# Performance work log

Measured on AMD Instinct MI355X. Metric: run time of the kernel, lower is better.

Reference implementation:

```python
import jax, jax.numpy as jnp
import numpy as np
import math

HEAD_DIM = 128

def _rope(t, cos, sin):
    # t: [B, S, H, D]; cos/sin: [S, D//2]; rotates consecutive pairs (view_as_complex semantics)
    B, S, H, D = t.shape
    t2 = t.reshape(B, S, H, D // 2, 2)
    t0, t1 = t2[..., 0], t2[..., 1]
    c = cos[None, :, None, :]
    s = sin[None, :, None, :]
    r0 = t0 * c - t1 * s
    r1 = t0 * s + t1 * c
    return jnp.stack([r0, r1], axis=-1).reshape(B, S, H, D)

def setup_inputs() -> dict:
    key = jax.random.key(0)
    ks = jax.random.split(key, 8)
    B, S, dim = 32, 1, 4096
    n_q, n_kv, hd = 32, 8, HEAD_DIM
    max_seq = 2048
    start_pos = 2047
    x = jax.random.normal(ks[0], (B, S, dim), dtype=jnp.float32)
    wq = jax.random.normal(ks[1], (n_q * hd, dim), dtype=jnp.float32) * 0.02
    wk = jax.random.normal(ks[2], (n_kv * hd, dim), dtype=jnp.float32) * 0.02
    wv = jax.random.normal(ks[3], (n_kv * hd, dim), dtype=jnp.float32) * 0.02
    wo = jax.random.normal(ks[4], (dim, n_q * hd), dtype=jnp.float32) * 0.02
    # real RoPE frequencies at positions [start_pos, start_pos+S)
    inv_freq = 1.0 / (10000.0 ** (np.arange(0, hd, 2, dtype=np.float32) / hd))  # [hd//2]
    pos = np.arange(start_pos, start_pos + S, dtype=np.float32)[:, None]
    angles = pos * inv_freq[None, :]  # [S, hd//2]
    freqs_cos = jnp.asarray(np.cos(angles), dtype=jnp.float32)
    freqs_sin = jnp.asarray(np.sin(angles), dtype=jnp.float32)
    cache_k = jax.random.normal(ks[5], (B, max_seq, n_kv, hd), dtype=jnp.float32)
    cache_v = jax.random.normal(ks[6], (B, max_seq, n_kv, hd), dtype=jnp.float32)
    return {"x": x, "wq": wq, "wk": wk, "wv": wv, "wo": wo,
            "freqs_cos": freqs_cos, "freqs_sin": freqs_sin,
            "cache_k": cache_k, "cache_v": cache_v, "start_pos": start_pos}

def reference(x, wq, wk, wv, wo, freqs_cos, freqs_sin, cache_k, cache_v, start_pos):
    B, S, dim = x.shape
    hd = HEAD_DIM
    n_q = wq.shape[0] // hd
    n_kv = wk.shape[0] // hd
    rep = n_q // n_kv
    q = (x @ wq.T).reshape(B, S, n_q, hd)
    k = (x @ wk.T).reshape(B, S, n_kv, hd)
    v = (x @ wv.T).reshape(B, S, n_kv, hd)
    q = _rope(q, freqs_cos, freqs_sin)
    k = _rope(k, freqs_cos, freqs_sin)
    # KV-cache update (start_pos is a static Python int)
    ck = jax.lax.dynamic_update_slice(cache_k, k, (0, start_pos, 0, 0))
    cv = jax.lax.dynamic_update_slice(cache_v, v, (0, start_pos, 0, 0))
    T = start_pos + S
    kk = ck[:, :T]  # [B, T, n_kv, hd]
    vv = cv[:, :T]
    # GQA without materializing repeated heads: q head h -> (g=h//rep, r=h%rep)
    qg = q.reshape(B, S, n_kv, rep, hd)
    scores = jnp.einsum('bsgrd,btgd->bgrst', qg, kk) / math.sqrt(hd)
    attn = jax.nn.softmax(scores, axis=-1)
    out = jnp.einsum('bgrst,btgd->bsgrd', attn, vv).reshape(B, S, n_q * hd)
    return out @ wo.T
```

## Files before the change

### kernel.cpp

```cpp
#include <hip/hip_runtime.h>
#include <hip/hip_bf16.h>


typedef __bf16 bf16x8_t __attribute__((ext_vector_type(8)));
typedef float f32x4_t __attribute__((ext_vector_type(4)));

#define KDIM 4096
#define NTOT_QKV 6144
#define NTOT_O 4096
#define NKV 8
#define HD 128

static __device__ inline bf16x8_t cvt8(const float4* p) {
  float4 u = p[0], v = p[1];
  bf16x8_t r;
  r[0] = (__bf16)u.x; r[1] = (__bf16)u.y; r[2] = (__bf16)u.z; r[3] = (__bf16)u.w;
  r[4] = (__bf16)v.x; r[5] = (__bf16)v.y; r[6] = (__bf16)v.z; r[7] = (__bf16)v.w;
  return r;
}

__global__ __launch_bounds__(256) void qkv_mfma(
    const float* __restrict__ X,
    const float* __restrict__ Wq,
    const float* __restrict__ Wk,
    const float* __restrict__ Wv,
    float* __restrict__ part)
{
  int wid  = (blockIdx.x * blockDim.x + threadIdx.x) >> 6;
  int lane = threadIdx.x & 63;
  const int ntiles = NTOT_QKV >> 4;
  int nt = wid % ntiles;
  int kc = wid / ntiles;
  int k0 = kc << 9;
  int rr = lane & 15;
  int quad = lane >> 4;

  int ng = nt * 16 + rr;
  const float* Wrow;
  if (ng < 4096)      Wrow = Wq + (size_t)ng * KDIM;
  else if (ng < 5120) Wrow = Wk + (size_t)(ng - 4096) * KDIM;
  else                Wrow = Wv + (size_t)(ng - 5120) * KDIM;

  const float4* pa0 = (const float4*)(X + (size_t)rr * KDIM + k0) + quad * 2;
  const float4* pa1 = (const float4*)(X + (size_t)(rr + 16) * KDIM + k0) + quad * 2;
  const float4* pbv = (const float4*)(Wrow + k0) + quad * 2;

  f32x4_t acc0 = {0.f, 0.f, 0.f, 0.f};
  f32x4_t acc1 = {0.f, 0.f, 0.f, 0.f};
  #pragma unroll 4
  for (int s = 0; s < 16; ++s) {
    bf16x8_t a0 = cvt8(pa0 + s * 8);
    bf16x8_t a1 = cvt8(pa1 + s * 8);
    bf16x8_t bb = cvt8(pbv + s * 8);
    acc0 = __builtin_amdgcn_mfma_f32_16x16x32_bf16(a0, bb, acc0, 0, 0, 0);
    acc1 = __builtin_amdgcn_mfma_f32_16x16x32_bf16(a1, bb, acc1, 0, 0, 0);
  }
  float* p = part + (size_t)kc * 32 * NTOT_QKV + ng;
  #pragma unroll
  for (int i = 0; i < 4; ++i) {
    int m = quad * 4 + i;
    p[(size_t)m * NTOT_QKV] = acc0[i];
    p[(size_t)(m + 16) * NTOT_QKV] = acc1[i];
  }
}

__global__ __launch_bounds__(256) void reduce_rope(
    const float* __restrict__ part,
    const float* __restrict__ cosv,
    const float* __restrict__ sinv,
    float* __restrict__ qws,
    float* __restrict__ kws,
    float* __restrict__ vws)
{
  int idx = blockIdx.x * blockDim.x + threadIdx.x;
  int b = idx / 3072;
  int rem = idx - b * 3072;
  int n0 = rem * 2;
  const float* p = part + (size_t)b * NTOT_QKV + n0;
  float s0 = 0.f, s1 = 0.f;
  #pragma unroll
  for (int c = 0; c < 8; ++c) {
    s0 += p[(size_t)c * 32 * NTOT_QKV + 0];
    s1 += p[(size_t)c * 32 * NTOT_QKV + 1];
  }
  if (n0 < 4096) {
    int d = n0 & 127; int j = d >> 1;
    float cf = cosv[j], sf = sinv[j];
    qws[(size_t)b * 4096 + n0]     = s0 * cf - s1 * sf;
    qws[(size_t)b * 4096 + n0 + 1] = s0 * sf + s1 * cf;
  } else if (n0 < 5120) {
    int nn = n0 - 4096;
    int d = nn & 127; int j = d >> 1;
    float cf = cosv[j], sf = sinv[j];
    kws[(size_t)b * 1024 + nn]     = s0 * cf - s1 * sf;
    kws[(size_t)b * 1024 + nn + 1] = s0 * sf + s1 * cf;
  } else {
    int nn = n0 - 5120;
    vws[(size_t)b * 1024 + nn]     = s0;
    vws[(size_t)b * 1024 + nn + 1] = s1;
  }
}

__global__ __launch_bounds__(256) void attn_partial(
    const float* __restrict__ cache_k,
    const float* __restrict__ cache_v,
    const float* __restrict__ qws,
    const float* __restrict__ kws,
    const float* __restrict__ vws,
    float* __restrict__ part)
{
  int bidx = blockIdx.x;
  int c = bidx & 7;
  int pair = bidx >> 3;
  int h = pair & 7, b = pair >> 3;
  int tid = threadIdx.x;

  __shared__ float4 kbuf[2048];
  __shared__ float4 q4l[128];
  __shared__ float4 pl4[256];

  if (tid < 128)
    q4l[tid] = ((const float4*)(qws + (size_t)b * 4096 + (size_t)h * 512))[tid];

  const int r  = tid >> 6;
  const int tl = tid & 63;
  const int sw = tl & 7;

  float s[4];
  #pragma unroll
  for (int st = 0; st < 4; ++st) {
    int t0 = c * 256 + st * 64;
    float4 tmp[8];
    #pragma unroll
    for (int j = 0; j < 8; ++j) {
      int f = tid + j * 256;
      int row = f >> 5, col = f & 31;
      const float4* src;
      if (c == 7 && st == 3 && row == 63)
        src = (const float4*)(kws + ((size_t)b * NKV + h) * HD) + col;
      else
        src = (const float4*)(cache_k + (((size_t)b * 2048 + t0 + row) * NKV + h) * HD) + col;
      tmp[j] = *src;
    }
    #pragma unroll
    for (int j = 0; j < 8; ++j) {
      int f = tid + j * 256;
      int row = f >> 5, col = f & 31;
      kbuf[row * 32 + (col ^ (row & 7))] = tmp[j];
    }
    __syncthreads();
    const float4* kr = kbuf + tl * 32;
    float acc = 0.f;
    #pragma unroll 8
    for (int d4 = 0; d4 < 32; ++d4) {
      float4 q4 = q4l[r * 32 + d4];
      float4 k4 = kr[d4 ^ sw];
      acc += q4.x * k4.x + q4.y * k4.y + q4.z * k4.z + q4.w * k4.w;
    }
    s[st] = acc * 0.088388347648318447f;
    __syncthreads();
  }

  float m = fmaxf(fmaxf(s[0], s[1]), fmaxf(s[2], s[3]));
  #pragma unroll
  for (int off = 32; off; off >>= 1) m = fmaxf(m, __shfl_xor(m, off, 64));
  float lsum = 0.f;
  float* plf = (float*)pl4;
  #pragma unroll
  for (int st = 0; st < 4; ++st) {
    float p = __expf(s[st] - m);
    lsum += p;
    plf[(st * 64 + tl) * 4 + r] = p;
  }
  #pragma unroll
  for (int off = 32; off; off >>= 1) lsum += __shfl_xor(lsum, off, 64);

  float* pb = part + (size_t)bidx * 520;
  if (tl == 0) { pb[r] = m; pb[4 + r] = lsum; }
  __syncthreads();

  int d4 = tid & 31;
  int g  = tid >> 3 >> 2;
  float4 a0 = {0,0,0,0}, a1 = {0,0,0,0}, a2 = {0,0,0,0}, a3 = {0,0,0,0};
  const float4* vp = (const float4*)(cache_v +
      (((size_t)b * 2048 + c * 256 + g * 32) * NKV + h) * HD) + d4;
  #pragma unroll 4
  for (int i = 0; i < 32; ++i) {
    float4 v4 = vp[(size_t)i * 256];
    float4 pv = pl4[g * 32 + i];
    a0.x += pv.x * v4.x; a0.y += pv.x * v4.y; a0.z += pv.x * v4.z; a0.w += pv.x * v4.w;
    a1.x += pv.y * v4.x; a1.y += pv.y * v4.y; a1.z += pv.y * v4.z; a1.w += pv.y * v4.w;
    a2.x += pv.z * v4.x; a2.y += pv.z * v4.y; a2.z += pv.z * v4.z; a2.w += pv.z * v4.w;
    a3.x += pv.w * v4.x; a3.y += pv.w * v4.y; a3.z += pv.w * v4.z; a3.w += pv.w * v4.w;
  }
  if (c == 7 && g == 7) {
    float4 vold = vp[(size_t)31 * 256];
    float4 vn = ((const float4*)(vws + ((size_t)b * NKV + h) * HD))[d4];
    float4 dv; dv.x = vn.x - vold.x; dv.y = vn.y - vold.y;
    dv.z = vn.z - vold.z; dv.w = vn.w - vold.w;
    float4 pv = pl4[255];
    a0.x += pv.x * dv.x; a0.y += pv.x * dv.y; a0.z += pv.x * dv.z; a0.w += pv.x * dv.w;
    a1.x += pv.y * dv.x; a1.y += pv.y * dv.y; a1.z += pv.y * dv.z; a1.w += pv.y * dv.w;
    a2.x += pv.z * dv.x; a2.y += pv.z * dv.y; a2.z += pv.z * dv.z; a2.w += pv.z * dv.w;
    a3.x += pv.w * dv.x; a3.y += pv.w * dv.y; a3.z += pv.w * dv.z; a3.w += pv.w * dv.w;
  }
  float4* pred = kbuf;
  pred[(g * 4 + 0) * 32 + d4] = a0;
  pred[(g * 4 + 1) * 32 + d4] = a1;
  pred[(g * 4 + 2) * 32 + d4] = a2;
  pred[(g * 4 + 3) * 32 + d4] = a3;
  __syncthreads();

  if (tid < 128) {
    int r2 = tid >> 5, dd = tid & 31;
    float4 o = {0,0,0,0};
    #pragma unroll
    for (int gg = 0; gg < 8; ++gg) {
      float4 t4 = pred[(gg * 4 + r2) * 32 + dd];
      o.x += t4.x; o.y += t4.y; o.z += t4.z; o.w += t4.w;
    }
    *(float4*)(pb + 8 + r2 * 128 + dd * 4) = o;
  }
}

__global__ __launch_bounds__(128) void attn_combine(
    const float* __restrict__ part,
    float* __restrict__ attn_out)
{
  int pair = blockIdx.x;
  int h = pair & 7, b = pair >> 3;
  int d = threadIdx.x;
  const float* pb = part + (size_t)pair * 8 * 520;
  #pragma unroll
  for (int r = 0; r < 4; ++r) {
    float M = -1e30f;
    #pragma unroll
    for (int c = 0; c < 8; ++c) M = fmaxf(M, pb[c * 520 + r]);
    float L = 0.f, o = 0.f;
    #pragma unroll
    for (int c = 0; c < 8; ++c) {
      float w = __expf(pb[c * 520 + r] - M);
      L += w * pb[c * 520 + 4 + r];
      o += w * pb[c * 520 + 8 + r * 128 + d];
    }
    attn_out[(size_t)b * 4096 + (h * 4 + r) * 128 + d] = o / L;
  }
}

__global__ __launch_bounds__(256) void oproj_mfma(
    const float* __restrict__ X,
    const float* __restrict__ W,
    float* __restrict__ part)
{
  int wid  = (blockIdx.x * blockDim.x + threadIdx.x) >> 6;
  int lane = threadIdx.x & 63;
  const int ntiles = NTOT_O >> 4;
  int nt = wid % ntiles;
  int kc = wid / ntiles;
  int k0 = kc << 9;
  int rr = lane & 15;
  int quad = lane >> 4;
  int ng = nt * 16 + rr;

  const float4* pa0 = (const float4*)(X + (size_t)rr * KDIM + k0) + quad * 2;
  const float4* pa1 = (const float4*)(X + (size_t)(rr + 16) * KDIM + k0) + quad * 2;
  const float4* pbv = (const float4*)(W + (size_t)ng * KDIM + k0) + quad * 2;

  f32x4_t acc0 = {0.f, 0.f, 0.f, 0.f};
  f32x4_t acc1 = {0.f, 0.f, 0.f, 0.f};
  #pragma unroll 4
  for (int s = 0; s < 16; ++s) {
    bf16x8_t a0 = cvt8(pa0 + s * 8);
    bf16x8_t a1 = cvt8(pa1 + s * 8);
    bf16x8_t bb = cvt8(pbv + s * 8);
    acc0 = __builtin_amdgcn_mfma_f32_16x16x32_bf16(a0, bb, acc0, 0, 0, 0);
    acc1 = __builtin_amdgcn_mfma_f32_16x16x32_bf16(a1, bb, acc1, 0, 0, 0);
  }
  float* p = part + (size_t)kc * 32 * NTOT_O + ng;
  #pragma unroll
  for (int i = 0; i < 4; ++i) {
    int m = quad * 4 + i;
    p[(size_t)m * NTOT_O] = acc0[i];
    p[(size_t)(m + 16) * NTOT_O] = acc1[i];
  }
}

__global__ __launch_bounds__(256) void oproj_reduce(
    const float* __restrict__ part,
    float* __restrict__ out)
{
  int i = blockIdx.x * blockDim.x + threadIdx.x;
  float s = 0.f;
  #pragma unroll
  for (int c = 0; c < 8; ++c) s += part[(size_t)c * 131072 + i];
  out[i] = s;
}

extern "C" void kernel_launch(void* const* d_in, const int* in_sizes, int n_in,
                              void* d_out, int out_size, void* d_ws, size_t ws_size,
                              hipStream_t stream) {
  const float* x  = (const float*)d_in[0];
  const float* wq = (const float*)d_in[1];
  const float* wk = (const float*)d_in[2];
  const float* wv = (const float*)d_in[3];
  const float* wo = (const float*)d_in[4];
  const float* fc = (const float*)d_in[5];
  const float* fs = (const float*)d_in[6];
  const float* ck = (const float*)d_in[7];
  const float* cv = (const float*)d_in[8];

  char* ws = (char*)d_ws;
  float* part_qkv = (float*)(ws + 0);
  float* qws      = (float*)(ws + 6291456);
  float* kws      = (float*)(ws + 6815744);
  float* vws      = (float*)(ws + 6946816);
  float* part_at  = (float*)(ws + 7077888);
  float* attn_out = (float*)(ws + 11337728);
  float* part_o   = (float*)(ws + 0);

  qkv_mfma<<<768, 256, 0, stream>>>(x, wq, wk, wv, part_qkv);
  reduce_rope<<<384, 256, 0, stream>>>(part_qkv, fc, fs, qws, kws, vws);
  attn_partial<<<2048, 256, 0, stream>>>(ck, cv, qws, kws, vws, part_at);
  attn_combine<<<256, 128, 0, stream>>>(part_at, attn_out);
  oproj_mfma<<<512, 256, 0, stream>>>(attn_out, wo, part_o);
  oproj_reduce<<<512, 256, 0, stream>>>(part_o, (float*)d_out);
}
```

Measured before the change: 642.7 us.

## Pre-cast activations to bf16, double-buffer weight tiles in LDS, prefetch K cache

Adds a cast_x kernel and has attn_combine write bf16, so both GEMMs read bf16 activations instead of converting fp32 in every wave. The QKV and O-projection GEMMs now give each block a 64-column tile and stage converted weights through a double-buffered, swizzled LDS tile. The next K-step's global loads are issued before the current MFMAs, so load latency overlaps with compute. The attention kernel similarly prefetches the next K-cache tile into registers while computing on the current one. The costs are one extra kernel launch, more barriers, and higher register and LDS use.

```diff
diff --git a/kernel.cpp b/kernel.cpp
--- a/kernel.cpp
+++ b/kernel.cpp
@@ -11,50 +11,96 @@
 #define NKV 8
 #define HD 128
 
-static __device__ inline bf16x8_t cvt8(const float4* p) {
-  float4 u = p[0], v = p[1];
+static __device__ inline bf16x8_t cvt8r(float4 u, float4 v) {
   bf16x8_t r;
   r[0] = (__bf16)u.x; r[1] = (__bf16)u.y; r[2] = (__bf16)u.z; r[3] = (__bf16)u.w;
   r[4] = (__bf16)v.x; r[5] = (__bf16)v.y; r[6] = (__bf16)v.z; r[7] = (__bf16)v.w;
   return r;
 }
 
+__global__ __launch_bounds__(256) void cast_x(const float* __restrict__ X,
+                                              __bf16* __restrict__ Xb) {
+  int i = blockIdx.x * 256 + threadIdx.x;
+  const float4* p = (const float4*)(X + (size_t)i * 8);
+  *(bf16x8_t*)(Xb + (size_t)i * 8) = cvt8r(p[0], p[1]);
+}
+
 __global__ __launch_bounds__(256) void qkv_mfma(
-    const float* __restrict__ X,
+    const __bf16* __restrict__ Xb,
     const float* __restrict__ Wq,
     const float* __restrict__ Wk,
     const float* __restrict__ Wv,
     float* __restrict__ part)
 {
-  int wid  = (blockIdx.x * blockDim.x + threadIdx.x) >> 6;
-  int lane = threadIdx.x & 63;
-  const int ntiles = NTOT_QKV >> 4;
-  int nt = wid % ntiles;
-  int kc = wid / ntiles;
+  int nt = blockIdx.x % 96;
+  int kc = blockIdx.x / 96;
   int k0 = kc << 9;
-  int rr = lane & 15;
-  int quad = lane >> 4;
-
-  int ng = nt * 16 + rr;
-  const float* Wrow;
-  if (ng < 4096)      Wrow = Wq + (size_t)ng * KDIM;
-  else if (ng < 5120) Wrow = Wk + (size_t)(ng - 4096) * KDIM;
-  else                Wrow = Wv + (size_t)(ng - 5120) * KDIM;
-
-  const float4* pa0 = (const float4*)(X + (size_t)rr * KDIM + k0) + quad * 2;
-  const float4* pa1 = (const float4*)(X + (size_t)(rr + 16) * KDIM + k0) + quad * 2;
-  const float4* pbv = (const float4*)(Wrow + k0) + quad * 2;
+  int tid = threadIdx.x;
+  int w = tid >> 6, lane = tid & 63;
+  int rr = lane & 15, quad = lane >> 4;
+
+  int ngbase = nt * 64;
+  const float* Wbase;
+  if (nt < 64)      Wbase = Wq + (size_t)ngbase * KDIM;
+  else if (nt < 80) Wbase = Wk + (size_t)(ngbase - 4096) * KDIM;
+  else              Wbase = Wv + (size_t)(ngbase - 5120) * KDIM;
+
+  __shared__ bf16x8_t wl[2][512];
+
+  int f8a = tid, f8b = tid + 256;
+  int ra = f8a >> 3, ca = f8a & 7;
+  int rb = f8b >> 3, cb = f8b & 7;
+  const float4* ga = (const float4*)(Wbase + (size_t)ra * KDIM + k0 + ca * 8);
+  const float4* gb = (const float4*)(Wbase + (size_t)rb * KDIM + k0 + cb * 8);
+  int sa = ra * 8 + (ca ^ (ra & 7));
+  int sb = rb * 8 + (cb ^ (rb & 7));
+
+  const __bf16* xa0 = Xb + (size_t)rr * KDIM + k0 + quad * 8;
+  const __bf16* xa1 = Xb + (size_t)(rr + 16) * KDIM + k0 + quad * 8;
+  int brow = w * 16 + rr;
+  int bs0 = brow * 8 + ((quad)     ^ (brow & 7));
+  int bs1 = brow * 8 + ((quad + 4) ^ (brow & 7));
 
   f32x4_t acc0 = {0.f, 0.f, 0.f, 0.f};
   f32x4_t acc1 = {0.f, 0.f, 0.f, 0.f};
-  #pragma unroll 4
-  for (int s = 0; s < 16; ++s) {
-    bf16x8_t a0 = cvt8(pa0 + s * 8);
-    bf16x8_t a1 = cvt8(pa1 + s * 8);
-    bf16x8_t bb = cvt8(pbv + s * 8);
-    acc0 = __builtin_amdgcn_mfma_f32_16x16x32_bf16(a0, bb, acc0, 0, 0, 0);
-    acc1 = __builtin_amdgcn_mfma_f32_16x16x32_bf16(a1, bb, acc1, 0, 0, 0);
-  }
+
+  float4 wa0 = ga[0], wa1 = ga[1], wb0 = gb[0], wb1 = gb[1];
+  bf16x8_t A00 = *(const bf16x8_t*)(xa0);
+  bf16x8_t A10 = *(const bf16x8_t*)(xa1);
+  bf16x8_t A01 = *(const bf16x8_t*)(xa0 + 32);
+  bf16x8_t A11 = *(const bf16x8_t*)(xa1 + 32);
+  wl[0][sa] = cvt8r(wa0, wa1);
+  wl[0][sb] = cvt8r(wb0, wb1);
+  __syncthreads();
+
+  #pragma unroll
+  for (int s = 0; s < 8; ++s) {
+    int cur = s & 1;
+    float4 nwa0, nwa1, nwb0, nwb1;
+    bf16x8_t N00, N10, N01, N11;
+    if (s < 7) {
+      nwa0 = ga[(s + 1) * 16];     nwa1 = ga[(s + 1) * 16 + 1];
+      nwb0 = gb[(s + 1) * 16];     nwb1 = gb[(s + 1) * 16 + 1];
+      N00 = *(const bf16x8_t*)(xa0 + (s + 1) * 64);
+      N10 = *(const bf16x8_t*)(xa1 + (s + 1) * 64);
+      N01 = *(const bf16x8_t*)(xa0 + (s + 1) * 64 + 32);
+      N11 = *(const bf16x8_t*)(xa1 + (s + 1) * 64 + 32);
+    }
+    bf16x8_t b0 = wl[cur][bs0];
+    bf16x8_t b1 = wl[cur][bs1];
+    acc0 = __builtin_amdgcn_mfma_f32_16x16x32_bf16(A00, b0, acc0, 0, 0, 0);
+    acc1 = __builtin_amdgcn_mfma_f32_16x16x32_bf16(A10, b0, acc1, 0, 0, 0);
+    acc0 = __builtin_amdgcn_mfma_f32_16x16x32_bf16(A01, b1, acc0, 0, 0, 0);
+    acc1 = __builtin_amdgcn_mfma_f32_16x16x32_bf16(A11, b1, acc1, 0, 0, 0);
+    if (s < 7) {
+      wl[cur ^ 1][sa] = cvt8r(nwa0, nwa1);
+      wl[cur ^ 1][sb] = cvt8r(nwb0, nwb1);
+      A00 = N00; A10 = N10; A01 = N01; A11 = N11;
+    }
+    __syncthreads();
+  }
+
+  int ng = ngbase + w * 16 + rr;
   float* p = part + (size_t)kc * 32 * NTOT_QKV + ng;
   #pragma unroll
   for (int i = 0; i < 4; ++i) {
@@ -126,22 +172,19 @@
   const int tl = tid & 63;
   const int sw = tl & 7;
 
+  const float* kcb = cache_k + (((size_t)b * 2048 + c * 256) * NKV + h) * HD;
+  const float4* knew = (const float4*)(kws + ((size_t)b * NKV + h) * HD);
+
+  float4 tmp[8];
+  #pragma unroll
+  for (int j = 0; j < 8; ++j) {
+    int f = tid + j * 256, row = f >> 5, col = f & 31;
+    tmp[j] = *((const float4*)(kcb + (size_t)row * (NKV * HD)) + col);
+  }
+
   float s[4];
   #pragma unroll
   for (int st = 0; st < 4; ++st) {
-    int t0 = c * 256 + st * 64;
-    float4 tmp[8];
-    #pragma unroll
-    for (int j = 0; j < 8; ++j) {
-      int f = tid + j * 256;
-      int row = f >> 5, col = f & 31;
-      const float4* src;
-      if (c == 7 && st == 3 && row == 63)
-        src = (const float4*)(kws + ((size_t)b * NKV + h) * HD) + col;
-      else
-        src = (const float4*)(cache_k + (((size_t)b * 2048 + t0 + row) * NKV + h) * HD) + col;
-      tmp[j] = *src;
-    }
     #pragma unroll
     for (int j = 0; j < 8; ++j) {
       int f = tid + j * 256;
@@ -149,6 +192,18 @@
       kbuf[row * 32 + (col ^ (row & 7))] = tmp[j];
     }
     __syncthreads();
+    if (st < 3) {
+      #pragma unroll
+      for (int j = 0; j < 8; ++j) {
+        int f = tid + j * 256, row = f >> 5, col = f & 31;
+        const float4* src;
+        if (c == 7 && st == 2 && row == 63)
+          src = knew + col;
+        else
+          src = (const float4*)(kcb + (size_t)((st + 1) * 64 + row) * (NKV * HD)) + col;
+        tmp[j] = *src;
+      }
+    }
     const float4* kr = kbuf + tl * 32;
     float acc = 0.f;
     #pragma unroll 8
@@ -180,7 +235,7 @@
   __syncthreads();
 
   int d4 = tid & 31;
-  int g  = tid >> 3 >> 2;
+  int g  = tid >> 5;
   float4 a0 = {0,0,0,0}, a1 = {0,0,0,0}, a2 = {0,0,0,0}, a3 = {0,0,0,0};
   const float4* vp = (const float4*)(cache_v +
       (((size_t)b * 2048 + c * 256 + g * 32) * NKV + h) * HD) + d4;
@@ -225,7 +280,7 @@
 
 __global__ __launch_bounds__(128) void attn_combine(
     const float* __restrict__ part,
-    float* __restrict__ attn_out)
+    __bf16* __restrict__ aobf)
 {
   int pair = blockIdx.x;
   int h = pair & 7, b = pair >> 3;
@@ -243,39 +298,81 @@
       L += w * pb[c * 520 + 4 + r];
       o += w * pb[c * 520 + 8 + r * 128 + d];
     }
-    attn_out[(size_t)b * 4096 + (h * 4 + r) * 128 + d] = o / L;
+    aobf[(size_t)b * 4096 + (h * 4 + r) * 128 + d] = (__bf16)(o / L);
   }
 }
 
 __global__ __launch_bounds__(256) void oproj_mfma(
-    const float* __restrict__ X,
+    const __bf16* __restrict__ Xb,
     const float* __restrict__ W,
     float* __restrict__ part)
 {
-  int wid  = (blockIdx.x * blockDim.x + threadIdx.x) >> 6;
-  int lane = threadIdx.x & 63;
-  const int ntiles = NTOT_O >> 4;
-  int nt = wid % ntiles;
-  int kc = wid / ntiles;
+  int nt = blockIdx.x & 63;
+  int kc = blockIdx.x >> 6;
   int k0 = kc << 9;
-  int rr = lane & 15;
-  int quad = lane >> 4;
-  int ng = nt * 16 + rr;
-
-  const float4* pa0 = (const float4*)(X + (size_t)rr * KDIM + k0) + quad * 2;
-  const float4* pa1 = (const float4*)(X + (size_t)(rr + 16) * KDIM + k0) + quad * 2;
-  const float4* pbv = (const float4*)(W + (size_t)ng * KDIM + k0) + quad * 2;
+  int tid = threadIdx.x;
+  int w = tid >> 6, lane = tid & 63;
+  int rr = lane & 15, quad = lane >> 4;
+
+  int ngbase = nt * 64;
+  const float* Wbase = W + (size_t)ngbase * KDIM;
+
+  __shared__ bf16x8_t wl[2][512];
+
+  int f8a = tid, f8b = tid + 256;
+  int ra = f8a >> 3, ca = f8a & 7;
+  int rb = f8b >> 3, cb = f8b & 7;
+  const float4* ga = (const float4*)(Wbase + (size_t)ra * KDIM + k0 + ca * 8);
+  const float4* gb = (const float4*)(Wbase + (size_t)rb * KDIM + k0 + cb * 8);
+  int sa = ra * 8 + (ca ^ (ra & 7));
+  int sb = rb * 8 + (cb ^ (rb & 7));
+
+  const __bf16* xa0 = Xb + (size_t)rr * KDIM + k0 + quad * 8;
+  const __bf16* xa1 = Xb + (size_t)(rr + 16) * KDIM + k0 + quad * 8;
+  int brow = w * 16 + rr;
+  int bs0 = brow * 8 + ((quad)     ^ (brow & 7));
+  int bs1 = brow * 8 + ((quad + 4) ^ (brow & 7));
 
   f32x4_t acc0 = {0.f, 0.f, 0.f, 0.f};
   f32x4_t acc1 = {0.f, 0.f, 0.f, 0.f};
-  #pragma unroll 4
-  for (int s = 0; s < 16; ++s) {
-    bf16x8_t a0 = cvt8(pa0 + s * 8);
-    bf16x8_t a1 = cvt8(pa1 + s * 8);
-    bf16x8_t bb = cvt8(pbv + s * 8);
-    acc0 = __builtin_amdgcn_mfma_f32_16x16x32_bf16(a0, bb, acc0, 0, 0, 0);
-    acc1 = __builtin_amdgcn_mfma_f32_16x16x32_bf16(a1, bb, acc1, 0, 0, 0);
-  }
+
+  float4 wa0 = ga[0], wa1 = ga[1], wb0 = gb[0], wb1 = gb[1];
+  bf16x8_t A00 = *(const bf16x8_t*)(xa0);
+  bf16x8_t A10 = *(const bf16x8_t*)(xa1);
+  bf16x8_t A01 = *(const bf16x8_t*)(xa0 + 32);
+  bf16x8_t A11 = *(const bf16x8_t*)(xa1 + 32);
+  wl[0][sa] = cvt8r(wa0, wa1);
+  wl[0][sb] = cvt8r(wb0, wb1);
+  __syncthreads();
+
+  #pragma unroll
+  for (int s = 0; s < 8; ++s) {
+    int cur = s & 1;
+    float4 nwa0, nwa1, nwb0, nwb1;
+    bf16x8_t N00, N10, N01, N11;
+    if (s < 7) {
+      nwa0 = ga[(s + 1) * 16];     nwa1 = ga[(s + 1) * 16 + 1];
+      nwb0 = gb[(s + 1) * 16];     nwb1 = gb[(s + 1) * 16 + 1];
+      N00 = *(const bf16x8_t*)(xa0 + (s + 1) * 64);
+      N10 = *(const bf16x8_t*)(xa1 + (s + 1) * 64);
+      N01 = *(const bf16x8_t*)(xa0 + (s + 1) * 64 + 32);
+      N11 = *(const bf16x8_t*)(xa1 + (s + 1) * 64 + 32);
+    }
+    bf16x8_t b0 = wl[cur][bs0];
+    bf16x8_t b1 = wl[cur][bs1];
+    acc0 = __builtin_amdgcn_mfma_f32_16x16x32_bf16(A00, b0, acc0, 0, 0, 0);
+    acc1 = __builtin_amdgcn_mfma_f32_16x16x32_bf16(A10, b0, acc1, 0, 0, 0);
+    acc0 = __builtin_amdgcn_mfma_f32_16x16x32_bf16(A01, b1, acc0, 0, 0, 0);
+    acc1 = __builtin_amdgcn_mfma_f32_16x16x32_bf16(A11, b1, acc1, 0, 0, 0);
+    if (s < 7) {
+      wl[cur ^ 1][sa] = cvt8r(nwa0, nwa1);
+      wl[cur ^ 1][sb] = cvt8r(nwb0, nwb1);
+      A00 = N00; A10 = N10; A01 = N01; A11 = N11;
+    }
+    __syncthreads();
+  }
+
+  int ng = ngbase + w * 16 + rr;
   float* p = part + (size_t)kc * 32 * NTOT_O + ng;
   #pragma unroll
   for (int i = 0; i < 4; ++i) {
@@ -310,18 +407,20 @@
   const float* cv = (const float*)d_in[8];
 
   char* ws = (char*)d_ws;
-  float* part_qkv = (float*)(ws + 0);
-  float* qws      = (float*)(ws + 6291456);
-  float* kws      = (float*)(ws + 6815744);
-  float* vws      = (float*)(ws + 6946816);
-  float* part_at  = (float*)(ws + 7077888);
-  float* attn_out = (float*)(ws + 11337728);
-  float* part_o   = (float*)(ws + 0);
-
-  qkv_mfma<<<768, 256, 0, stream>>>(x, wq, wk, wv, part_qkv);
+  float*  part_qkv = (float*)(ws + 0);
+  float*  qws      = (float*)(ws + 6291456);
+  float*  kws      = (float*)(ws + 6815744);
+  float*  vws      = (float*)(ws + 6946816);
+  float*  part_at  = (float*)(ws + 7077888);
+  __bf16* xbf      = (__bf16*)(ws + 11337728);
+  __bf16* aobf     = (__bf16*)(ws + 11599872);
+  float*  part_o   = (float*)(ws + 0);
+
+  cast_x<<<64, 256, 0, stream>>>(x, xbf);
+  qkv_mfma<<<768, 256, 0, stream>>>(xbf, wq, wk, wv, part_qkv);
   reduce_rope<<<384, 256, 0, stream>>>(part_qkv, fc, fs, qws, kws, vws);
   attn_partial<<<2048, 256, 0, stream>>>(ck, cv, qws, kws, vws, part_at);
-  attn_combine<<<256, 128, 0, stream>>>(part_at, attn_out);
-  oproj_mfma<<<512, 256, 0, stream>>>(attn_out, wo, part_o);
+  attn_combine<<<256, 128, 0, stream>>>(part_at, aobf);
+  oproj_mfma<<<512, 256, 0, stream>>>(aobf, wo, part_o);
   oproj_reduce<<<512, 256, 0, stream>>>(part_o, (float*)d_out);
 }
```

New measurement: 678.3 us. +5.5%, slower.
